# Performance work log

Hardware: AMD Instinct MI355X
Metric: run time of the kernel (lower is better)

## Reference

```python
import jax, jax.numpy as jnp
import numpy as np

B, T, H, HEADS, K, L = 64, 512, 512, 4, 3, 16
R, A = 256, 9


def _pe(t, h):
    pos = np.arange(t)[:, None].astype(np.float32)
    div = np.exp(-np.log(10000.0) * np.arange(0, h, 2).astype(np.float32) / h)
    pe = np.zeros((t, h), np.float32)
    pe[:, 0::2] = np.sin(pos * div)
    pe[:, 1::2] = np.cos(pos * div)
    return jnp.asarray(pe)


def _ln(x, g, b, eps=1e-5):
    m = x.mean(-1, keepdims=True)
    v = ((x - m) ** 2).mean(-1, keepdims=True)
    return (x - m) * jax.lax.rsqrt(v + eps) * g + b


def _dwconv(x, k):
    # x [B,T,C], k [K,C]: depthwise temporal conv, SAME padding
    kern = k[:, None, :]  # [K, 1, C] in WIO layout, groups = C
    return jax.lax.conv_general_dilated(
        x, kern, (1,), 'SAME',
        dimension_numbers=('NWC', 'WIO', 'NWC'),
        feature_group_count=x.shape[-1])


def setup_inputs():
    key = jax.random.key(0)
    ks = jax.random.split(key, 16)
    n = lambda i, shape, s=0.02: jax.random.normal(ks[i], shape, jnp.float32) * s
    return dict(
        rssi=jax.random.normal(ks[0], (B, T, R), jnp.float32),
        accl=jax.random.normal(ks[1], (B, T, A), jnp.float32),
        rssi_W=n(2, (R, H)), rssi_b=jnp.zeros((H,), jnp.float32),
        accl_W=n(3, (A, H)), accl_b=jnp.zeros((H,), jnp.float32),
        conv_r=n(4, (K, H), 0.1), conv_a=n(5, (K, H), 0.1),
        Wq=n(6, (H, H)), Wk=n(7, (H, H)), Wv=n(8, (H, H)), Wo=n(9, (H, H)),
        ln1_g=jnp.ones((H,), jnp.float32), ln1_b=jnp.zeros((H,), jnp.float32),
        W1=n(10, (H, 4 * H)), b1=jnp.zeros((4 * H,), jnp.float32),
        W2=n(11, (4 * H, H)), b2=jnp.zeros((H,), jnp.float32),
        ln2_g=jnp.ones((H,), jnp.float32), ln2_b=jnp.zeros((H,), jnp.float32),
        loc_W=n(12, (H, L)), loc_b=jnp.zeros((L,), jnp.float32),
        start_trans=n(13, (L,), 0.1), end_trans=n(14, (L,), 0.1),
        trans=n(15, (L, L), 0.1),
    )


def _emissions(rssi, accl, rssi_W, rssi_b, accl_W, accl_b, conv_r, conv_a,
               Wq, Wk, Wv, Wo, ln1_g, ln1_b, W1, b1, W2, b2, ln2_g, ln2_b,
               loc_W, loc_b):
    t, h = rssi.shape[1], rssi_W.shape[1]
    pe = _pe(t, h)
    r = rssi @ rssi_W + rssi_b + pe                   # [B,T,H]
    a = accl @ accl_W + accl_b + pe                   # [B,T,H]
    x = _dwconv(r, conv_r) + _dwconv(a, conv_a)       # dual-conv fusion
    b_, t_, _ = x.shape
    dh = h // HEADS
    q = (x @ Wq).reshape(b_, t_, HEADS, dh)
    k = (x @ Wk).reshape(b_, t_, HEADS, dh)
    v = (x @ Wv).reshape(b_, t_, HEADS, dh)
    logits = jnp.einsum('bqhd,bkhd->bhqk', q, k) / jnp.sqrt(jnp.float32(dh))
    attn = jax.nn.softmax(logits, axis=-1)
    o = jnp.einsum('bhqk,bkhd->bqhd', attn, v).reshape(b_, t_, h) @ Wo
    x = _ln(x + o, ln1_g, ln1_b)
    f = jax.nn.relu(x @ W1 + b1) @ W2 + b2
    x = _ln(x + f, ln2_g, ln2_b)
    return x @ loc_W + loc_b                          # emissions [B,T,L]


def _viterbi(em, start_trans, end_trans, trans):
    # torchcrf-style Viterbi decode (batch_first, full-length sequences)
    score0 = start_trans + em[:, 0]                   # [B,L]

    def step(score, em_t):
        tot = score[:, :, None] + trans[None] + em_t[:, None, :]  # [B,L,L]
        return tot.max(axis=1), tot.argmax(axis=1)

    score, hist = jax.lax.scan(step, score0, jnp.swapaxes(em[:, 1:], 0, 1))
    final = score + end_trans
    last = jnp.argmax(final, axis=-1)                 # [B]
    best = jnp.max(final, axis=-1)                    # [B] best-path score

    def back(tag, h):
        prev = jnp.take_along_axis(h, tag[:, None], axis=1)[:, 0]
        return prev, prev

    _, path = jax.lax.scan(back, last, hist, reverse=True)
    tags = jnp.concatenate([path, last[None]], axis=0)  # [T,B]
    return jnp.swapaxes(tags, 0, 1).astype(jnp.int64), best


def reference(rssi, accl, rssi_W, rssi_b, accl_W, accl_b, conv_r, conv_a,
              Wq, Wk, Wv, Wo, ln1_g, ln1_b, W1, b1, W2, b2, ln2_g, ln2_b,
              loc_W, loc_b, start_trans, end_trans, trans):
    em = _emissions(rssi, accl, rssi_W, rssi_b, accl_W, accl_b, conv_r, conv_a,
                    Wq, Wk, Wv, Wo, ln1_g, ln1_b, W1, b1, W2, b2,
                    ln2_g, ln2_b, loc_W, loc_b)
    tags, _ = _viterbi(em, start_trans, end_trans, trans)
    return tags  # [B,T] int decoded locations
```

## Files before the change

### kernel.cpp

```cpp
#include <hip/hip_runtime.h>
#include <math.h>

constexpr int Bc = 64, Tc = 512, Hc = 512, HEADSc = 4, Lc = 16, Rc = 256, Ac = 9;
constexpr int DH = 128;

#define F_BIAS 1
#define F_PE   2
#define F_ADDC 4
#define F_RELU 8
#define F_DIV  16
#define F_QKV  32

using short8   = __attribute__((ext_vector_type(8)))  short;
using floatx16 = __attribute__((ext_vector_type(16))) float;
using ushort4v = __attribute__((ext_vector_type(4)))  unsigned short;

struct S3 { unsigned short h, m, l; };
__device__ inline S3 split3(float v)
{
    S3 r;
    unsigned u = __float_as_uint(v);
    r.h = (unsigned short)(u >> 16);
    float r1 = v - __uint_as_float(u & 0xffff0000u);
    unsigned u1 = __float_as_uint(r1);
    r.m = (unsigned short)(u1 >> 16);
    float r2 = r1 - __uint_as_float(u1 & 0xffff0000u);
    r.l = (unsigned short)(__float_as_uint(r2) >> 16);
    return r;
}

template<bool BSPLIT>
__global__ __launch_bounds__(256)
void mgemm(const float* __restrict__ A, const float* __restrict__ Bf,
           const unsigned short* __restrict__ Bsp, long long bPS,
           float* __restrict__ C, const float* __restrict__ bias,
           const float* __restrict__ pe,
           int M, int N, int K, int lda, int ldb, int ldc,
           long long s1A, long long s2A, long long s1B, long long s2B,
           long long s1C, long long s2C, float divv, int flags)
{
    int z = blockIdx.z, z1 = z >> 2, z2 = z & 3;
    A += (size_t)z1 * s1A + (size_t)z2 * s2A;
    if (!BSPLIT) Bf += (size_t)z1 * s1B + (size_t)z2 * s2B;
    C += (size_t)z1 * s1C + (size_t)z2 * s2C;

    __shared__ unsigned short Ah[128][40], Am[128][40], Al[128][40];
    __shared__ unsigned short Bh[128][40], Bm[128][40], Bl[128][40];

    int bm = blockIdx.y * 128, bn = blockIdx.x * 128;
    int tid = threadIdx.x;
    int lane = tid & 63, wave = tid >> 6;
    int wr = wave >> 1, wc = wave & 1;
    int l31 = lane & 31, khalf = lane >> 5;

    floatx16 acc[2][2];
    #pragma unroll
    for (int i = 0; i < 2; i++)
        #pragma unroll
        for (int j = 0; j < 2; j++)
            #pragma unroll
            for (int e = 0; e < 16; e++) acc[i][j][e] = 0.f;

    for (int k0 = 0; k0 < K; k0 += 32) {
        #pragma unroll
        for (int it = 0; it < 4; it++) {
            int s = tid + 256 * it;
            int mm = s >> 3, kc = (s & 7) << 2;
            float4 v = *(const float4*)(A + (size_t)(bm + mm) * lda + k0 + kc);
            ushort4v h, m, l;
            S3 s0 = split3(v.x); h[0] = s0.h; m[0] = s0.m; l[0] = s0.l;
            S3 s1 = split3(v.y); h[1] = s1.h; m[1] = s1.m; l[1] = s1.l;
            S3 s2 = split3(v.z); h[2] = s2.h; m[2] = s2.m; l[2] = s2.l;
            S3 s3 = split3(v.w); h[3] = s3.h; m[3] = s3.m; l[3] = s3.l;
            *(ushort4v*)&Ah[mm][kc] = h;
            *(ushort4v*)&Am[mm][kc] = m;
            *(ushort4v*)&Al[mm][kc] = l;
        }
        if (BSPLIT) {
            #pragma unroll
            for (int it = 0; it < 2; it++) {
                int s = tid + 256 * it;
                int nn = s >> 2, kc = (s & 3) << 3;
                size_t go = (size_t)(bn + nn) * ldb + k0 + kc;
                *(short8*)&Bh[nn][kc] = *(const short8*)(Bsp + go);
                *(short8*)&Bm[nn][kc] = *(const short8*)(Bsp + bPS + go);
                *(short8*)&Bl[nn][kc] = *(const short8*)(Bsp + 2 * bPS + go);
            }
        } else {
            #pragma unroll
            for (int it = 0; it < 4; it++) {
                int s = tid + 256 * it;
                int nn = s >> 3, kc = (s & 7) << 2;
                float4 v = *(const float4*)(Bf + (size_t)(bn + nn) * ldb + k0 + kc);
                ushort4v h, m, l;
                S3 s0 = split3(v.x); h[0] = s0.h; m[0] = s0.m; l[0] = s0.l;
                S3 s1 = split3(v.y); h[1] = s1.h; m[1] = s1.m; l[1] = s1.l;
                S3 s2 = split3(v.z); h[2] = s2.h; m[2] = s2.m; l[2] = s2.l;
                S3 s3 = split3(v.w); h[3] = s3.h; m[3] = s3.m; l[3] = s3.l;
                *(ushort4v*)&Bh[nn][kc] = h;
                *(ushort4v*)&Bm[nn][kc] = m;
                *(ushort4v*)&Bl[nn][kc] = l;
            }
        }
        __syncthreads();

        #pragma unroll
        for (int s = 0; s < 2; s++) {
            int ko = s * 16 + khalf * 8;
            short8 a0[2], a1[2], a2[2], b0[2], b1[2], b2[2];
            #pragma unroll
            for (int i = 0; i < 2; i++) {
                int ar = wr * 64 + i * 32 + l31;
                a0[i] = *(const short8*)&Ah[ar][ko];
                a1[i] = *(const short8*)&Am[ar][ko];
                a2[i] = *(const short8*)&Al[ar][ko];
                int br = wc * 64 + i * 32 + l31;
                b0[i] = *(const short8*)&Bh[br][ko];
                b1[i] = *(const short8*)&Bm[br][ko];
                b2[i] = *(const short8*)&Bl[br][ko];
            }
            #pragma unroll
            for (int i = 0; i < 2; i++)
                #pragma unroll
                for (int j = 0; j < 2; j++)
                    acc[i][j] = __builtin_amdgcn_mfma_f32_32x32x16_bf16(a0[i], b0[j], acc[i][j], 0, 0, 0);
            #pragma unroll
            for (int i = 0; i < 2; i++)
                #pragma unroll
                for (int j = 0; j < 2; j++)
                    acc[i][j] = __builtin_amdgcn_mfma_f32_32x32x16_bf16(a0[i], b1[j], acc[i][j], 0, 0, 0);
            #pragma unroll
            for (int i = 0; i < 2; i++)
                #pragma unroll
                for (int j = 0; j < 2; j++)
                    acc[i][j] = __builtin_amdgcn_mfma_f32_32x32x16_bf16(a1[i], b0[j], acc[i][j], 0, 0, 0);
            #pragma unroll
            for (int i = 0; i < 2; i++)
                #pragma unroll
                for (int j = 0; j < 2; j++)
                    acc[i][j] = __builtin_amdgcn_mfma_f32_32x32x16_bf16(a0[i], b2[j], acc[i][j], 0, 0, 0);
            #pragma unroll
            for (int i = 0; i < 2; i++)
                #pragma unroll
                for (int j = 0; j < 2; j++)
                    acc[i][j] = __builtin_amdgcn_mfma_f32_32x32x16_bf16(a2[i], b0[j], acc[i][j], 0, 0, 0);
            #pragma unroll
            for (int i = 0; i < 2; i++)
                #pragma unroll
                for (int j = 0; j < 2; j++)
                    acc[i][j] = __builtin_amdgcn_mfma_f32_32x32x16_bf16(a1[i], b1[j], acc[i][j], 0, 0, 0);
        }
        __syncthreads();
    }

    #pragma unroll
    for (int i = 0; i < 2; i++) {
        #pragma unroll
        for (int j = 0; j < 2; j++) {
            #pragma unroll
            for (int r = 0; r < 16; r++) {
                int m = bm + wr * 64 + i * 32 + (r & 3) + ((r >> 2) << 3) + (khalf << 2);
                int n = bn + wc * 64 + j * 32 + l31;
                float v = acc[i][j][r];
                if (flags & F_DIV)  v /= divv;
                if (flags & F_BIAS) v += bias[n];
                if (flags & F_PE)   v += pe[(size_t)(m & (Tc - 1)) * Hc + n];
                if (flags & F_QKV) {
                    long long gth = s1C;
                    if (n < 512) {
                        C[(size_t)m * 512 + n] = v;
                    } else if (n < 1024) {
                        C[gth + (size_t)m * 512 + (n - 512)] = v;
                    } else {
                        C[2 * gth + (size_t)(m >> 9) * (Tc * Hc)
                          + (size_t)(n - 1024) * Tc + (m & (Tc - 1))] = v;
                    }
                } else {
                    if (flags & F_ADDC) v += C[(size_t)m * ldc + n];
                    if (flags & F_RELU) v = fmaxf(v, 0.f);
                    C[(size_t)m * ldc + n] = v;
                }
            }
        }
    }
}

__global__ __launch_bounds__(256)
void wsplit_kernel(const float* __restrict__ W, unsigned short* __restrict__ out,
                   int K, int N, long long PS)
{
    __shared__ float t[64][65];
    int k0 = blockIdx.x * 64, n0 = blockIdx.y * 64;
    int tid = threadIdx.x;
    int c = tid & 63, r4 = tid >> 6;
    #pragma unroll
    for (int i = 0; i < 16; i++) {
        int r = r4 * 16 + i;
        t[r][c] = W[(size_t)(k0 + r) * N + n0 + c];
    }
    __syncthreads();
    #pragma unroll
    for (int i = 0; i < 16; i++) {
        int n = r4 * 16 + i;
        S3 s = split3(t[c][n]);
        size_t o = (size_t)(n0 + n) * K + k0 + c;
        out[o] = s.h; out[PS + o] = s.m; out[2 * PS + o] = s.l;
    }
}

__global__ void pe_kernel(float* __restrict__ pe)
{
    int idx = blockIdx.x * 256 + threadIdx.x;
    if (idx >= Tc * Hc) return;
    int t = idx >> 9, n = idx & (Hc - 1);
    int j = n >> 1;
    double div = exp(-log(10000.0) * (double)(2 * j) / (double)Hc);
    double arg = (double)t * div;
    pe[idx] = (float)((n & 1) ? cos(arg) : sin(arg));
}

__global__ __launch_bounds__(256)
void accl_kernel(const float* __restrict__ accl, const float* __restrict__ W,
                 const float* __restrict__ bias, const float* __restrict__ pe,
                 float* __restrict__ out)
{
    int idx = blockIdx.x * 256 + threadIdx.x;
    int n = idx & (Hc - 1);
    int m = idx >> 9;
    int t = m & (Tc - 1);
    const float* arow = accl + (size_t)m * Ac;
    float s = 0.f;
    #pragma unroll
    for (int i = 0; i < Ac; i++) s += arow[i] * W[i * Hc + n];
    s += bias[n];
    s += pe[t * Hc + n];
    out[idx] = s;
}

__global__ __launch_bounds__(256)
void dwconv_kernel(const float* __restrict__ r, const float* __restrict__ a,
                   const float* __restrict__ cr, const float* __restrict__ ca,
                   float* __restrict__ x)
{
    int idx = blockIdx.x * 256 + threadIdx.x;
    int c = idx & (Hc - 1);
    int m = idx >> 9;
    int t = m & (Tc - 1);
    float vr = r[idx] * cr[Hc + c];
    if (t > 0)      vr = r[idx - Hc] * cr[c] + vr;
    if (t < Tc - 1) vr = vr + r[idx + Hc] * cr[2 * Hc + c];
    float va = a[idx] * ca[Hc + c];
    if (t > 0)      va = a[idx - Hc] * ca[c] + va;
    if (t < Tc - 1) va = va + a[idx + Hc] * ca[2 * Hc + c];
    x[idx] = vr + va;
}

__global__ __launch_bounds__(256)
void softmax_kernel(float* __restrict__ L)
{
    size_t base = (size_t)blockIdx.x * 512;
    int tid = threadIdx.x;
    float v0 = L[base + tid], v1 = L[base + tid + 256];
    __shared__ float buf[256];
    buf[tid] = fmaxf(v0, v1);
    __syncthreads();
    for (int s = 128; s > 0; s >>= 1) {
        if (tid < s) buf[tid] = fmaxf(buf[tid], buf[tid + s]);
        __syncthreads();
    }
    float mx = buf[0];
    __syncthreads();
    float e0 = expf(v0 - mx), e1 = expf(v1 - mx);
    buf[tid] = e0 + e1;
    __syncthreads();
    for (int s = 128; s > 0; s >>= 1) {
        if (tid < s) buf[tid] += buf[tid + s];
        __syncthreads();
    }
    float sum = buf[0];
    L[base + tid] = e0 / sum;
    L[base + tid + 256] = e1 / sum;
}

__global__ __launch_bounds__(256)
void add_ln_kernel(const float* __restrict__ X, const float* __restrict__ Y,
                   const float* __restrict__ g, const float* __restrict__ bta,
                   float* __restrict__ out)
{
    size_t base = (size_t)blockIdx.x * 512;
    int tid = threadIdx.x;
    float v0 = X[base + tid] + Y[base + tid];
    float v1 = X[base + tid + 256] + Y[base + tid + 256];
    __shared__ float buf[256];
    buf[tid] = v0 + v1;
    __syncthreads();
    for (int s = 128; s > 0; s >>= 1) {
        if (tid < s) buf[tid] += buf[tid + s];
        __syncthreads();
    }
    float mean = buf[0] / 512.f;
    __syncthreads();
    float d0 = v0 - mean, d1 = v1 - mean;
    buf[tid] = d0 * d0 + d1 * d1;
    __syncthreads();
    for (int s = 128; s > 0; s >>= 1) {
        if (tid < s) buf[tid] += buf[tid + s];
        __syncthreads();
    }
    float var = buf[0] / 512.f;
    float rs = 1.0f / sqrtf(var + 1e-5f);
    out[base + tid]       = d0 * rs * g[tid] + bta[tid];
    out[base + tid + 256] = d1 * rs * g[tid + 256] + bta[tid + 256];
}

__global__ __launch_bounds__(256)
void em_kernel(const float* __restrict__ X, const float* __restrict__ W,
               const float* __restrict__ bias, float* __restrict__ out)
{
    __shared__ float Wl[8192];
    int tid = threadIdx.x;
    #pragma unroll
    for (int i = 0; i < 32; i++) Wl[tid + 256 * i] = W[tid + 256 * i];
    __syncthreads();
    int r = tid >> 4, l = tid & 15;
    const float* xr = X + ((size_t)blockIdx.x * 16 + r) * Hc;
    float s = 0.f;
    #pragma unroll 8
    for (int k = 0; k < Hc; k++) s += xr[k] * Wl[k * Lc + l];
    s += bias[l];
    out[((size_t)blockIdx.x * 16 + r) * Lc + l] = s;
}

__global__ __launch_bounds__(64)
void viterbi_kernel(const float* __restrict__ em, const float* __restrict__ st,
                    const float* __restrict__ et, const float* __restrict__ trans,
                    int* __restrict__ out)
{
    int b = blockIdx.x;
    int tid = threadIdx.x;
    __shared__ float ems[2][64][Lc];
    __shared__ float sc[2][Lc];
    __shared__ unsigned char hist[Tc - 1][Lc];
    float trcol[Lc];
    if (tid < Lc) {
        #pragma unroll
        for (int i = 0; i < Lc; i++) trcol[i] = trans[i * Lc + tid];
    }
    const float* emb = em + (size_t)b * Tc * Lc;
    {
        const float4* src = (const float4*)emb;
        float4* dst = (float4*)&ems[0][0][0];
        #pragma unroll
        for (int i = 0; i < 4; i++) dst[tid + 64 * i] = src[tid + 64 * i];
    }
    __syncthreads();
    if (tid < Lc) sc[0][tid] = st[tid] + ems[0][0][tid];
    __syncthreads();
    int cur = 0;
    for (int c = 0; c < 8; c++) {
        if (c < 7) {
            const float4* src = (const float4*)(emb + (size_t)(c + 1) * 64 * Lc);
            float4* dst = (float4*)&ems[(c + 1) & 1][0][0];
            #pragma unroll
            for (int i = 0; i < 4; i++) dst[tid + 64 * i] = src[tid + 64 * i];
        }
        int tt0 = (c == 0) ? 1 : 0;
        for (int tt = tt0; tt < 64; tt++) {
            int t = c * 64 + tt;
            if (tid < Lc) {
                float e = ems[c & 1][tt][tid];
                float v[Lc];
                #pragma unroll
                for (int i = 0; i < Lc; i++) v[i] = (sc[cur][i] + trcol[i]) + e;
                float bv[8]; int bi[8];
                #pragma unroll
                for (int i = 0; i < 8; i++) {
                    bool ge = v[2 * i] >= v[2 * i + 1];
                    bv[i] = ge ? v[2 * i] : v[2 * i + 1];
                    bi[i] = ge ? 2 * i : 2 * i + 1;
                }
                #pragma unroll
                for (int i = 0; i < 4; i++) {
                    bool ge = bv[2 * i] >= bv[2 * i + 1];
                    bv[i] = ge ? bv[2 * i] : bv[2 * i + 1];
                    bi[i] = ge ? bi[2 * i] : bi[2 * i + 1];
                }
                #pragma unroll
                for (int i = 0; i < 2; i++) {
                    bool ge = bv[2 * i] >= bv[2 * i + 1];
                    bv[i] = ge ? bv[2 * i] : bv[2 * i + 1];
                    bi[i] = ge ? bi[2 * i] : bi[2 * i + 1];
                }
                bool ge = bv[0] >= bv[1];
                sc[cur ^ 1][tid] = ge ? bv[0] : bv[1];
                hist[t - 1][tid] = (unsigned char)(ge ? bi[0] : bi[1]);
            }
            __syncthreads();
            cur ^= 1;
        }
    }
    if (tid == 0) {
        float best = sc[cur][0] + et[0];
        int tag = 0;
        #pragma unroll
        for (int j = 1; j < Lc; j++) {
            float v = sc[cur][j] + et[j];
            if (v > best) { best = v; tag = j; }
        }
        out[(size_t)b * Tc + (Tc - 1)] = tag;
        for (int t = Tc - 2; t >= 0; t--) {
            tag = hist[t][tag];
            out[(size_t)b * Tc + t] = tag;
        }
    }
}

__global__ void diag_kernel(int* __restrict__ out, int n, int val)
{
    int i = blockIdx.x * 256 + threadIdx.x;
    if (i < n) out[i] = val;
}

extern "C" void kernel_launch(void* const* d_in, const int* in_sizes, int n_in,
                              void* d_out, int out_size, void* d_ws, size_t ws_size,
                              hipStream_t stream)
{
    const float* rssi   = (const float*)d_in[0];
    const float* accl   = (const float*)d_in[1];
    const float* rssi_W = (const float*)d_in[2];
    const float* rssi_b = (const float*)d_in[3];
    const float* accl_W = (const float*)d_in[4];
    const float* accl_b = (const float*)d_in[5];
    const float* conv_r = (const float*)d_in[6];
    const float* conv_a = (const float*)d_in[7];
    const float* Wq     = (const float*)d_in[8];
    const float* Wk     = (const float*)d_in[9];
    const float* Wv     = (const float*)d_in[10];
    const float* Wo     = (const float*)d_in[11];
    const float* ln1_g  = (const float*)d_in[12];
    const float* ln1_b  = (const float*)d_in[13];
    const float* W1     = (const float*)d_in[14];
    const float* b1     = (const float*)d_in[15];
    const float* W2     = (const float*)d_in[16];
    const float* b2     = (const float*)d_in[17];
    const float* ln2_g  = (const float*)d_in[18];
    const float* ln2_b  = (const float*)d_in[19];
    const float* loc_W  = (const float*)d_in[20];
    const float* loc_b  = (const float*)d_in[21];
    const float* start_trans = (const float*)d_in[22];
    const float* end_trans   = (const float*)d_in[23];
    const float* trans       = (const float*)d_in[24];

    const int M = Bc * Tc;
    const size_t S = (size_t)M * Hc;
    const size_t TH = (size_t)Tc * Hc;
    const long long TT = (long long)Tc * Tc;
    const float sq = sqrtf((float)DH);
    dim3 blk(256);

    const size_t WBUF_SH = 9830400ull;
    const size_t WBUF_F  = WBUF_SH / 2;
    size_t total_f = ws_size / sizeof(float);
    size_t work_min = (size_t)M * 128;
    if (total_f < 2 * S + WBUF_F + TH + work_min) {
        diag_kernel<<<dim3((out_size + 255) / 256), blk, 0, stream>>>(
            (int*)d_out, out_size, 1000000 + (int)(ws_size >> 20));
        return;
    }

    float* bufX = (float*)d_ws;
    float* bufY = bufX + S;
    unsigned short* wbuf  = (unsigned short*)(bufY + S);
    unsigned short* rssiT = wbuf;
    unsigned short* qkvT  = wbuf + 393216;
    unsigned short* WoT   = wbuf + 2752512;
    unsigned short* W1T   = wbuf + 3538944;
    unsigned short* W2T   = wbuf + 6684672;
    float* pe_buf = (float*)(wbuf + WBUF_SH);
    float* work = pe_buf + TH;
    size_t work_n = total_f - 2 * S - WBUF_F - TH;

    int Ge = 1;
    for (int g = 64; g >= 1; g >>= 1) if ((size_t)g * TH <= work_n) { Ge = g; break; }
    int Ga = 1;
    for (int g = 64; g >= 1; g >>= 1) if (8ull * g * TH <= work_n) { Ga = g; break; }
    int Nc = 128;
    for (int n = 2048; n >= 128; n >>= 1) if ((size_t)M * n <= work_n) { Nc = n; break; }

    pe_kernel<<<dim3((Tc * Hc + 255) / 256), blk, 0, stream>>>(pe_buf);
    wsplit_kernel<<<dim3(Rc / 64, Hc / 64), blk, 0, stream>>>(rssi_W, rssiT, Rc, Hc, 131072LL);
    wsplit_kernel<<<dim3(8, 8),  blk, 0, stream>>>(Wq, qkvT,          512, 512, 786432LL);
    wsplit_kernel<<<dim3(8, 8),  blk, 0, stream>>>(Wk, qkvT + 262144, 512, 512, 786432LL);
    wsplit_kernel<<<dim3(8, 8),  blk, 0, stream>>>(Wv, qkvT + 524288, 512, 512, 786432LL);
    wsplit_kernel<<<dim3(8, 8),  blk, 0, stream>>>(Wo, WoT, 512, 512, 262144LL);
    wsplit_kernel<<<dim3(8, 32), blk, 0, stream>>>(W1, W1T, 512, 2048, 1048576LL);
    wsplit_kernel<<<dim3(32, 8), blk, 0, stream>>>(W2, W2T, 2048, 512, 1048576LL);

    accl_kernel<<<dim3(M * (Hc / 256)), blk, 0, stream>>>(accl, accl_W, accl_b, pe_buf, bufY);
    for (int g0 = 0; g0 < Bc; g0 += Ge) {
        int rows = Ge * Tc;
        mgemm<true><<<dim3(Hc / 128, rows / 128, 1), blk, 0, stream>>>(
            rssi + (size_t)g0 * Tc * Rc, nullptr, rssiT, 131072LL,
            work, rssi_b, pe_buf,
            rows, Hc, Rc, Rc, Rc, Hc,
            0, 0, 0, 0, 0, 0, 1.f, F_BIAS | F_PE);
        dwconv_kernel<<<dim3(rows * (Hc / 256)), blk, 0, stream>>>(
            work, bufY + (size_t)g0 * TH, conv_r, conv_a, bufX + (size_t)g0 * TH);
    }

    for (int g0 = 0; g0 < Bc; g0 += Ga) {
        int rows = Ga * Tc;
        long long gth = (long long)Ga * TH;
        float* qg = work;
        float* kg = work + gth;
        float* vg = work + 2 * gth;
        float* og = work + 3 * gth;
        float* lg = work + 4 * gth;
        mgemm<true><<<dim3(1536 / 128, rows / 128, 1), blk, 0, stream>>>(
            bufX + (size_t)g0 * TH, nullptr, qkvT, 786432LL,
            qg, nullptr, nullptr,
            rows, 1536, Hc, Hc, 512, 0,
            0, 0, 0, 0, gth, 0, 1.f, F_QKV);
        mgemm<false><<<dim3(Tc / 128, Tc / 128, Ga * HEADSc), blk, 0, stream>>>(
            qg, kg, nullptr, 0,
            lg, nullptr, nullptr,
            Tc, Tc, DH, Hc, Hc, Tc,
            (long long)TH, DH, (long long)TH, DH,
            (long long)HEADSc * TT, TT, sq, F_DIV);
        softmax_kernel<<<dim3(Ga * HEADSc * Tc), blk, 0, stream>>>(lg);
        mgemm<false><<<dim3(DH / 128, Tc / 128, Ga * HEADSc), blk, 0, stream>>>(
            lg, vg, nullptr, 0,
            og, nullptr, nullptr,
            Tc, DH, Tc, Tc, Tc, Hc,
            (long long)HEADSc * TT, TT,
            (long long)TH, (long long)DH * Tc,
            (long long)TH, DH, 1.f, 0);
        mgemm<true><<<dim3(Hc / 128, rows / 128, 1), blk, 0, stream>>>(
            og, nullptr, WoT, 262144LL,
            bufY + (size_t)g0 * TH, nullptr, nullptr,
            rows, Hc, Hc, Hc, 512, Hc,
            0, 0, 0, 0, 0, 0, 1.f, 0);
    }

    add_ln_kernel<<<dim3(M), blk, 0, stream>>>(bufX, bufY, ln1_g, ln1_b, bufX);

    int nChunks = 2048 / Nc;
    for (int c = 0; c < nChunks; c++) {
        mgemm<true><<<dim3(Nc / 128, M / 128, 1), blk, 0, stream>>>(
            bufX, nullptr, W1T + (size_t)c * Nc * 512, 1048576LL,
            work, b1 + c * Nc, nullptr,
            M, Nc, Hc, Hc, 512, Nc,
            0, 0, 0, 0, 0, 0, 1.f, F_BIAS | F_RELU);
        mgemm<true><<<dim3(Hc / 128, M / 128, 1), blk, 0, stream>>>(
            work, nullptr, W2T + (size_t)c * Nc, 1048576LL,
            bufY, b2, nullptr,
            M, Hc, Nc, Nc, 2048, Hc,
            0, 0, 0, 0, 0, 0, 1.f, (c == 0) ? F_BIAS : F_ADDC);
    }

    add_ln_kernel<<<dim3(M), blk, 0, stream>>>(bufX, bufY, ln2_g, ln2_b, bufX);

    em_kernel<<<dim3(M / 16), blk, 0, stream>>>(bufX, loc_W, loc_b, work);

    viterbi_kernel<<<dim3(Bc), dim3(64), 0, stream>>>(
        work, start_trans, end_trans, trans, (int*)d_out);
}
```

Baseline: 3.247 ms.

## Pre-split activations into bf16 triplets once and rewrite Viterbi with wave shuffles

Activations are now split into three bf16 planes by a separate pass or by the producing GEMM/softmax epilogue, so the GEMM mainloop only copies pre-split short8 tiles instead of repeating split3 on each tile. This removes redundant float-to-bf16x3 conversion in every block that re-reads the same A/B rows, at the cost of extra planes in workspace memory and changed chunking of the FFN and attention buffers. The Viterbi recursion now keeps scores in registers and uses wave shuffles, dropping the per-step __syncthreads.

```diff
diff --git a/kernel.cpp b/kernel.cpp
--- a/kernel.cpp
+++ b/kernel.cpp
@@ -4,16 +4,16 @@
 constexpr int Bc = 64, Tc = 512, Hc = 512, HEADSc = 4, Lc = 16, Rc = 256, Ac = 9;
 constexpr int DH = 128;
 
-#define F_BIAS 1
-#define F_PE   2
-#define F_ADDC 4
-#define F_RELU 8
-#define F_DIV  16
-#define F_QKV  32
+#define F_BIAS   1
+#define F_PE     2
+#define F_ADDC   4
+#define F_RELU   8
+#define F_DIV    16
+#define F_QKV    32
+#define F_SPLITC 64
 
 using short8   = __attribute__((ext_vector_type(8)))  short;
 using floatx16 = __attribute__((ext_vector_type(16))) float;
-using ushort4v = __attribute__((ext_vector_type(4)))  unsigned short;
 
 struct S3 { unsigned short h, m, l; };
 __device__ inline S3 split3(float v)
@@ -29,23 +29,26 @@
     return r;
 }
 
-template<bool BSPLIT>
-__global__ __launch_bounds__(256)
-void mgemm(const float* __restrict__ A, const float* __restrict__ Bf,
-           const unsigned short* __restrict__ Bsp, long long bPS,
-           float* __restrict__ C, const float* __restrict__ bias,
-           const float* __restrict__ pe,
-           int M, int N, int K, int lda, int ldb, int ldc,
-           long long s1A, long long s2A, long long s1B, long long s2B,
-           long long s1C, long long s2C, float divv, int flags)
+__global__ __launch_bounds__(256)
+void mgemm3(const unsigned short* __restrict__ Asp, long long aPS,
+            const unsigned short* __restrict__ Bsp, long long bPS,
+            float* __restrict__ C, unsigned short* __restrict__ Csp,
+            long long cPS,
+            const float* __restrict__ bias, const float* __restrict__ pe,
+            int M, int N, int K, int lda, int ldb, int ldc,
+            long long s1A, long long s2A, long long s1B, long long s2B,
+            long long s1C, long long s2C, float divv, int flags)
 {
     int z = blockIdx.z, z1 = z >> 2, z2 = z & 3;
-    A += (size_t)z1 * s1A + (size_t)z2 * s2A;
-    if (!BSPLIT) Bf += (size_t)z1 * s1B + (size_t)z2 * s2B;
-    C += (size_t)z1 * s1C + (size_t)z2 * s2C;
-
-    __shared__ unsigned short Ah[128][40], Am[128][40], Al[128][40];
-    __shared__ unsigned short Bh[128][40], Bm[128][40], Bl[128][40];
+    Asp += (size_t)z1 * s1A + (size_t)z2 * s2A;
+    Bsp += (size_t)z1 * s1B + (size_t)z2 * s2B;
+    if (!(flags & F_QKV)) {
+        if (C)   C   += (size_t)z1 * s1C + (size_t)z2 * s2C;
+        if (Csp) Csp += (size_t)z1 * s1C + (size_t)z2 * s2C;
+    }
+
+    __shared__ unsigned short As[3][128][40];
+    __shared__ unsigned short Bs[3][128][40];
 
     int bm = blockIdx.y * 128, bn = blockIdx.x * 128;
     int tid = threadIdx.x;
@@ -63,44 +66,17 @@
 
     for (int k0 = 0; k0 < K; k0 += 32) {
         #pragma unroll
-        for (int it = 0; it < 4; it++) {
+        for (int it = 0; it < 2; it++) {
             int s = tid + 256 * it;
-            int mm = s >> 3, kc = (s & 7) << 2;
-            float4 v = *(const float4*)(A + (size_t)(bm + mm) * lda + k0 + kc);
-            ushort4v h, m, l;
-            S3 s0 = split3(v.x); h[0] = s0.h; m[0] = s0.m; l[0] = s0.l;
-            S3 s1 = split3(v.y); h[1] = s1.h; m[1] = s1.m; l[1] = s1.l;
-            S3 s2 = split3(v.z); h[2] = s2.h; m[2] = s2.m; l[2] = s2.l;
-            S3 s3 = split3(v.w); h[3] = s3.h; m[3] = s3.m; l[3] = s3.l;
-            *(ushort4v*)&Ah[mm][kc] = h;
-            *(ushort4v*)&Am[mm][kc] = m;
-            *(ushort4v*)&Al[mm][kc] = l;
-        }
-        if (BSPLIT) {
-            #pragma unroll
-            for (int it = 0; it < 2; it++) {
-                int s = tid + 256 * it;
-                int nn = s >> 2, kc = (s & 3) << 3;
-                size_t go = (size_t)(bn + nn) * ldb + k0 + kc;
-                *(short8*)&Bh[nn][kc] = *(const short8*)(Bsp + go);
-                *(short8*)&Bm[nn][kc] = *(const short8*)(Bsp + bPS + go);
-                *(short8*)&Bl[nn][kc] = *(const short8*)(Bsp + 2 * bPS + go);
-            }
-        } else {
-            #pragma unroll
-            for (int it = 0; it < 4; it++) {
-                int s = tid + 256 * it;
-                int nn = s >> 3, kc = (s & 7) << 2;
-                float4 v = *(const float4*)(Bf + (size_t)(bn + nn) * ldb + k0 + kc);
-                ushort4v h, m, l;
-                S3 s0 = split3(v.x); h[0] = s0.h; m[0] = s0.m; l[0] = s0.l;
-                S3 s1 = split3(v.y); h[1] = s1.h; m[1] = s1.m; l[1] = s1.l;
-                S3 s2 = split3(v.z); h[2] = s2.h; m[2] = s2.m; l[2] = s2.l;
-                S3 s3 = split3(v.w); h[3] = s3.h; m[3] = s3.m; l[3] = s3.l;
-                *(ushort4v*)&Bh[nn][kc] = h;
-                *(ushort4v*)&Bm[nn][kc] = m;
-                *(ushort4v*)&Bl[nn][kc] = l;
-            }
+            int rr = s >> 2, kc = (s & 3) << 3;
+            size_t ga = (size_t)(bm + rr) * lda + k0 + kc;
+            *(short8*)&As[0][rr][kc] = *(const short8*)(Asp + ga);
+            *(short8*)&As[1][rr][kc] = *(const short8*)(Asp + aPS + ga);
+            *(short8*)&As[2][rr][kc] = *(const short8*)(Asp + 2 * aPS + ga);
+            size_t gb = (size_t)(bn + rr) * ldb + k0 + kc;
+            *(short8*)&Bs[0][rr][kc] = *(const short8*)(Bsp + gb);
+            *(short8*)&Bs[1][rr][kc] = *(const short8*)(Bsp + bPS + gb);
+            *(short8*)&Bs[2][rr][kc] = *(const short8*)(Bsp + 2 * bPS + gb);
         }
         __syncthreads();
 
@@ -111,13 +87,13 @@
             #pragma unroll
             for (int i = 0; i < 2; i++) {
                 int ar = wr * 64 + i * 32 + l31;
-                a0[i] = *(const short8*)&Ah[ar][ko];
-                a1[i] = *(const short8*)&Am[ar][ko];
-                a2[i] = *(const short8*)&Al[ar][ko];
+                a0[i] = *(const short8*)&As[0][ar][ko];
+                a1[i] = *(const short8*)&As[1][ar][ko];
+                a2[i] = *(const short8*)&As[2][ar][ko];
                 int br = wc * 64 + i * 32 + l31;
-                b0[i] = *(const short8*)&Bh[br][ko];
-                b1[i] = *(const short8*)&Bm[br][ko];
-                b2[i] = *(const short8*)&Bl[br][ko];
+                b0[i] = *(const short8*)&Bs[0][br][ko];
+                b1[i] = *(const short8*)&Bs[1][br][ko];
+                b2[i] = *(const short8*)&Bs[2][br][ko];
             }
             #pragma unroll
             for (int i = 0; i < 2; i++)
@@ -167,14 +143,18 @@
                 if (flags & F_PE)   v += pe[(size_t)(m & (Tc - 1)) * Hc + n];
                 if (flags & F_QKV) {
                     long long gth = s1C;
-                    if (n < 512) {
-                        C[(size_t)m * 512 + n] = v;
-                    } else if (n < 1024) {
-                        C[gth + (size_t)m * 512 + (n - 512)] = v;
-                    } else {
-                        C[2 * gth + (size_t)(m >> 9) * (Tc * Hc)
-                          + (size_t)(n - 1024) * Tc + (m & (Tc - 1))] = v;
-                    }
+                    S3 sp = split3(v);
+                    size_t o;
+                    if (n < 512)       o = (size_t)m * 512 + n;
+                    else if (n < 1024) o = 3 * gth + (size_t)m * 512 + (n - 512);
+                    else               o = 6 * gth + (size_t)(m >> 9) * (Tc * Hc)
+                                           + (size_t)(n - 1024) * 512 + (m & 511);
+                    Csp[o] = sp.h; Csp[gth + o] = sp.m; Csp[2 * gth + o] = sp.l;
+                } else if (flags & F_SPLITC) {
+                    if (flags & F_RELU) v = fmaxf(v, 0.f);
+                    S3 sp = split3(v);
+                    size_t o = (size_t)m * ldc + n;
+                    Csp[o] = sp.h; Csp[cPS + o] = sp.m; Csp[2 * cPS + o] = sp.l;
                 } else {
                     if (flags & F_ADDC) v += C[(size_t)m * ldc + n];
                     if (flags & F_RELU) v = fmaxf(v, 0.f);
@@ -183,6 +163,26 @@
             }
         }
     }
+}
+
+__global__ __launch_bounds__(256)
+void asplit_kernel(const float* __restrict__ X, unsigned short* __restrict__ out,
+                   long long PS, long long E)
+{
+    long long off = ((long long)blockIdx.x * 256 + threadIdx.x) * 8;
+    if (off >= E) return;
+    float4 v0 = *(const float4*)(X + off);
+    float4 v1 = *(const float4*)(X + off + 4);
+    short8 h, m, l;
+    float vv[8] = {v0.x, v0.y, v0.z, v0.w, v1.x, v1.y, v1.z, v1.w};
+    #pragma unroll
+    for (int i = 0; i < 8; i++) {
+        S3 s = split3(vv[i]);
+        h[i] = (short)s.h; m[i] = (short)s.m; l[i] = (short)s.l;
+    }
+    *(short8*)(out + off) = h;
+    *(short8*)(out + PS + off) = m;
+    *(short8*)(out + 2 * PS + off) = l;
 }
 
 __global__ __launch_bounds__(256)
@@ -256,7 +256,8 @@
 }
 
 __global__ __launch_bounds__(256)
-void softmax_kernel(float* __restrict__ L)
+void softmax_split_kernel(const float* __restrict__ L,
+                          unsigned short* __restrict__ Ps, long long PS)
 {
     size_t base = (size_t)blockIdx.x * 512;
     int tid = threadIdx.x;
@@ -278,8 +279,11 @@
         __syncthreads();
     }
     float sum = buf[0];
-    L[base + tid] = e0 / sum;
-    L[base + tid + 256] = e1 / sum;
+    float p0 = e0 / sum, p1 = e1 / sum;
+    S3 a = split3(p0), b = split3(p1);
+    Ps[base + tid] = a.h; Ps[PS + base + tid] = a.m; Ps[2 * PS + base + tid] = a.l;
+    Ps[base + tid + 256] = b.h; Ps[PS + base + tid + 256] = b.m;
+    Ps[2 * PS + base + tid + 256] = b.l;
 }
 
 __global__ __launch_bounds__(256)
@@ -338,14 +342,12 @@
 {
     int b = blockIdx.x;
     int tid = threadIdx.x;
+    int j = tid & 15;
     __shared__ float ems[2][64][Lc];
-    __shared__ float sc[2][Lc];
     __shared__ unsigned char hist[Tc - 1][Lc];
     float trcol[Lc];
-    if (tid < Lc) {
-        #pragma unroll
-        for (int i = 0; i < Lc; i++) trcol[i] = trans[i * Lc + tid];
-    }
+    #pragma unroll
+    for (int i = 0; i < Lc; i++) trcol[i] = trans[i * Lc + j];
     const float* emb = em + (size_t)b * Tc * Lc;
     {
         const float4* src = (const float4*)emb;
@@ -354,9 +356,7 @@
         for (int i = 0; i < 4; i++) dst[tid + 64 * i] = src[tid + 64 * i];
     }
     __syncthreads();
-    if (tid < Lc) sc[0][tid] = st[tid] + ems[0][0][tid];
-    __syncthreads();
-    int cur = 0;
+    float sc = st[j] + ems[0][0][j];
     for (int c = 0; c < 8; c++) {
         if (c < 7) {
             const float4* src = (const float4*)(emb + (size_t)(c + 1) * 64 * Lc);
@@ -367,46 +367,29 @@
         int tt0 = (c == 0) ? 1 : 0;
         for (int tt = tt0; tt < 64; tt++) {
             int t = c * 64 + tt;
-            if (tid < Lc) {
-                float e = ems[c & 1][tt][tid];
-                float v[Lc];
-                #pragma unroll
-                for (int i = 0; i < Lc; i++) v[i] = (sc[cur][i] + trcol[i]) + e;
-                float bv[8]; int bi[8];
-                #pragma unroll
-                for (int i = 0; i < 8; i++) {
-                    bool ge = v[2 * i] >= v[2 * i + 1];
-                    bv[i] = ge ? v[2 * i] : v[2 * i + 1];
-                    bi[i] = ge ? 2 * i : 2 * i + 1;
-                }
-                #pragma unroll
-                for (int i = 0; i < 4; i++) {
-                    bool ge = bv[2 * i] >= bv[2 * i + 1];
-                    bv[i] = ge ? bv[2 * i] : bv[2 * i + 1];
-                    bi[i] = ge ? bi[2 * i] : bi[2 * i + 1];
-                }
-                #pragma unroll
-                for (int i = 0; i < 2; i++) {
-                    bool ge = bv[2 * i] >= bv[2 * i + 1];
-                    bv[i] = ge ? bv[2 * i] : bv[2 * i + 1];
-                    bi[i] = ge ? bi[2 * i] : bi[2 * i + 1];
-                }
-                bool ge = bv[0] >= bv[1];
-                sc[cur ^ 1][tid] = ge ? bv[0] : bv[1];
-                hist[t - 1][tid] = (unsigned char)(ge ? bi[0] : bi[1]);
+            float e = ems[c & 1][tt][j];
+            float best = (__shfl(sc, 0) + trcol[0]) + e;
+            int bi = 0;
+            #pragma unroll
+            for (int i = 1; i < Lc; i++) {
+                float v = (__shfl(sc, i) + trcol[i]) + e;
+                if (v > best) { best = v; bi = i; }
             }
-            __syncthreads();
-            cur ^= 1;
-        }
-    }
+            sc = best;
+            if (tid < Lc) hist[t - 1][j] = (unsigned char)bi;
+        }
+        __syncthreads();
+    }
+    float fv = sc + et[j];
+    float bv = __shfl(fv, 0);
+    int tag = 0;
+    #pragma unroll
+    for (int i = 1; i < Lc; i++) {
+        float v = __shfl(fv, i);
+        if (v > bv) { bv = v; tag = i; }
+    }
+    __syncthreads();
     if (tid == 0) {
-        float best = sc[cur][0] + et[0];
-        int tag = 0;
-        #pragma unroll
-        for (int j = 1; j < Lc; j++) {
-            float v = sc[cur][j] + et[j];
-            if (v > best) { best = v; tag = j; }
-        }
         out[(size_t)b * Tc + (Tc - 1)] = tag;
         for (int t = Tc - 2; t >= 0; t--) {
             tag = hist[t][tag];
@@ -461,8 +444,7 @@
     const size_t WBUF_SH = 9830400ull;
     const size_t WBUF_F  = WBUF_SH / 2;
     size_t total_f = ws_size / sizeof(float);
-    size_t work_min = (size_t)M * 128;
-    if (total_f < 2 * S + WBUF_F + TH + work_min) {
+    if (total_f < 2 * S + WBUF_F + TH + (size_t)M * 128) {
         diag_kernel<<<dim3((out_size + 255) / 256), blk, 0, stream>>>(
             (int*)d_out, out_size, 1000000 + (int)(ws_size >> 20));
         return;
@@ -481,11 +463,21 @@
     size_t work_n = total_f - 2 * S - WBUF_F - TH;
 
     int Ge = 1;
-    for (int g = 64; g >= 1; g >>= 1) if ((size_t)g * TH <= work_n) { Ge = g; break; }
+    for (int g = 64; g >= 1; g >>= 1)
+        if ((size_t)g * (196608 + TH) <= work_n) { Ge = g; break; }
     int Ga = 1;
-    for (int g = 64; g >= 1; g >>= 1) if (8ull * g * TH <= work_n) { Ga = g; break; }
-    int Nc = 128;
-    for (int n = 2048; n >= 128; n >>= 1) if ((size_t)M * n <= work_n) { Nc = n; break; }
+    for (int g = 64; g >= 1; g >>= 1)
+        if (16ull * g * TH <= work_n) { Ga = g; break; }
+    int Mg = 1024, Nc = 512;
+    for (int mg = 32768; mg >= 1024; mg >>= 1) {
+        bool found = false;
+        for (int nc = 2048; nc >= 512; nc >>= 1) {
+            if (768ll * mg + (3ll * mg * nc) / 2 <= (long long)work_n) {
+                Mg = mg; Nc = nc; found = true; break;
+            }
+        }
+        if (found) break;
+    }
 
     pe_kernel<<<dim3((Tc * Hc + 255) / 256), blk, 0, stream>>>(pe_buf);
     wsplit_kernel<<<dim3(Rc / 64, Hc / 64), blk, 0, stream>>>(rssi_W, rssiT, Rc, Hc, 131072LL);
@@ -499,63 +491,79 @@
     accl_kernel<<<dim3(M * (Hc / 256)), blk, 0, stream>>>(accl, accl_W, accl_b, pe_buf, bufY);
     for (int g0 = 0; g0 < Bc; g0 += Ge) {
         int rows = Ge * Tc;
-        mgemm<true><<<dim3(Hc / 128, rows / 128, 1), blk, 0, stream>>>(
-            rssi + (size_t)g0 * Tc * Rc, nullptr, rssiT, 131072LL,
-            work, rssi_b, pe_buf,
+        long long rsPS = (long long)Ge * 131072;
+        unsigned short* rsS = (unsigned short*)work;
+        float* rbuf = work + (size_t)Ge * 196608;
+        asplit_kernel<<<dim3((unsigned)(3 * rsPS / 8 / 256 / 3 * 3 ? (rsPS / (8 * 256)) : 1)), blk, 0, stream>>>(
+            rssi + (size_t)g0 * Tc * Rc, rsS, rsPS, rsPS);
+        mgemm3<<<dim3(Hc / 128, rows / 128, 1), blk, 0, stream>>>(
+            rsS, rsPS, rssiT, 131072LL,
+            rbuf, nullptr, 0, rssi_b, pe_buf,
             rows, Hc, Rc, Rc, Rc, Hc,
             0, 0, 0, 0, 0, 0, 1.f, F_BIAS | F_PE);
         dwconv_kernel<<<dim3(rows * (Hc / 256)), blk, 0, stream>>>(
-            work, bufY + (size_t)g0 * TH, conv_r, conv_a, bufX + (size_t)g0 * TH);
+            rbuf, bufY + (size_t)g0 * TH, conv_r, conv_a, bufX + (size_t)g0 * TH);
     }
 
     for (int g0 = 0; g0 < Bc; g0 += Ga) {
-        int rows = Ga * Tc;
-        long long gth = (long long)Ga * TH;
-        float* qg = work;
-        float* kg = work + gth;
-        float* vg = work + 2 * gth;
-        float* og = work + 3 * gth;
-        float* lg = work + 4 * gth;
-        mgemm<true><<<dim3(1536 / 128, rows / 128, 1), blk, 0, stream>>>(
-            bufX + (size_t)g0 * TH, nullptr, qkvT, 786432LL,
-            qg, nullptr, nullptr,
+        int g = Ga;
+        int rows = g * Tc;
+        long long gth = (long long)g * TH;
+        unsigned short* qkvS = (unsigned short*)work;
+        unsigned short* xsS  = qkvS + 9 * gth;
+        float* lg = work + 6 * gth;
+        unsigned short* PsS = (unsigned short*)(work + 10 * gth);
+        asplit_kernel<<<dim3((unsigned)(gth / (8 * 256))), blk, 0, stream>>>(
+            bufX + (size_t)g0 * TH, xsS, gth, gth);
+        mgemm3<<<dim3(1536 / 128, rows / 128, 1), blk, 0, stream>>>(
+            xsS, gth, qkvT, 786432LL,
+            nullptr, qkvS, 0, nullptr, nullptr,
             rows, 1536, Hc, Hc, 512, 0,
             0, 0, 0, 0, gth, 0, 1.f, F_QKV);
-        mgemm<false><<<dim3(Tc / 128, Tc / 128, Ga * HEADSc), blk, 0, stream>>>(
-            qg, kg, nullptr, 0,
-            lg, nullptr, nullptr,
-            Tc, Tc, DH, Hc, Hc, Tc,
+        mgemm3<<<dim3(Tc / 128, Tc / 128, g * HEADSc), blk, 0, stream>>>(
+            qkvS, gth, qkvS + 3 * gth, gth,
+            lg, nullptr, 0, nullptr, nullptr,
+            Tc, Tc, DH, 512, 512, Tc,
             (long long)TH, DH, (long long)TH, DH,
             (long long)HEADSc * TT, TT, sq, F_DIV);
-        softmax_kernel<<<dim3(Ga * HEADSc * Tc), blk, 0, stream>>>(lg);
-        mgemm<false><<<dim3(DH / 128, Tc / 128, Ga * HEADSc), blk, 0, stream>>>(
-            lg, vg, nullptr, 0,
-            og, nullptr, nullptr,
-            Tc, DH, Tc, Tc, Tc, Hc,
+        softmax_split_kernel<<<dim3(g * HEADSc * Tc), blk, 0, stream>>>(
+            lg, PsS, 4 * gth);
+        mgemm3<<<dim3(DH / 128, Tc / 128, g * HEADSc), blk, 0, stream>>>(
+            PsS, 4 * gth, qkvS + 6 * gth, gth,
+            nullptr, xsS, gth, nullptr, nullptr,
+            Tc, DH, Tc, 512, 512, 512,
             (long long)HEADSc * TT, TT,
-            (long long)TH, (long long)DH * Tc,
-            (long long)TH, DH, 1.f, 0);
-        mgemm<true><<<dim3(Hc / 128, rows / 128, 1), blk, 0, stream>>>(
-            og, nullptr, WoT, 262144LL,
-            bufY + (size_t)g0 * TH, nullptr, nullptr,
-            rows, Hc, Hc, Hc, 512, Hc,
+            (long long)TH, 65536LL,
+            (long long)TH, 128LL, 1.f, F_SPLITC);
+        mgemm3<<<dim3(Hc / 128, rows / 128, 1), blk, 0, stream>>>(
+            xsS, gth, WoT, 262144LL,
+            bufY + (size_t)g0 * TH, nullptr, 0, nullptr, nullptr,
+            rows, Hc, Hc, 512, 512, Hc,
             0, 0, 0, 0, 0, 0, 1.f, 0);
     }
 
     add_ln_kernel<<<dim3(M), blk, 0, stream>>>(bufX, bufY, ln1_g, ln1_b, bufX);
 
     int nChunks = 2048 / Nc;
-    for (int c = 0; c < nChunks; c++) {
-        mgemm<true><<<dim3(Nc / 128, M / 128, 1), blk, 0, stream>>>(
-            bufX, nullptr, W1T + (size_t)c * Nc * 512, 1048576LL,
-            work, b1 + c * Nc, nullptr,
-            M, Nc, Hc, Hc, 512, Nc,
-            0, 0, 0, 0, 0, 0, 1.f, F_BIAS | F_RELU);
-        mgemm<true><<<dim3(Hc / 128, M / 128, 1), blk, 0, stream>>>(
-            work, nullptr, W2T + (size_t)c * Nc, 1048576LL,
-            bufY, b2, nullptr,
-            M, Hc, Nc, Nc, 2048, Hc,
-            0, 0, 0, 0, 0, 0, 1.f, (c == 0) ? F_BIAS : F_ADDC);
+    for (int mg0 = 0; mg0 < M; mg0 += Mg) {
+        long long x1PS = (long long)Mg * 512;
+        unsigned short* x1S = (unsigned short*)work;
+        unsigned short* hS  = x1S + 3 * x1PS;
+        long long hPS = (long long)Mg * Nc;
+        asplit_kernel<<<dim3((unsigned)(x1PS / (8 * 256))), blk, 0, stream>>>(
+            bufX + (size_t)mg0 * 512, x1S, x1PS, x1PS);
+        for (int c = 0; c < nChunks; c++) {
+            mgemm3<<<dim3(Nc / 128, Mg / 128, 1), blk, 0, stream>>>(
+                x1S, x1PS, W1T + (size_t)c * Nc * 512, 1048576LL,
+                nullptr, hS, hPS, b1 + c * Nc, nullptr,
+                Mg, Nc, Hc, 512, 512, Nc,
+                0, 0, 0, 0, 0, 0, 1.f, F_BIAS | F_RELU | F_SPLITC);
+            mgemm3<<<dim3(Hc / 128, Mg / 128, 1), blk, 0, stream>>>(
+                hS, hPS, W2T + (size_t)c * Nc, 1048576LL,
+                bufY + (size_t)mg0 * 512, nullptr, 0, b2, nullptr,
+                Mg, Hc, Nc, Nc, 2048, Hc,
+                0, 0, 0, 0, 0, 0, 1.f, (c == 0) ? F_BIAS : F_ADDC);
+        }
     }
 
     add_ln_kernel<<<dim3(M), blk, 0, stream>>>(bufX, bufY, ln2_g, ln2_b, bufX);
```

New measurement: 4.747 ms. 46.2% more time.
